# Performance work log

Hardware: AMD Instinct MI355X
Metric: run time of the kernel (lower is better)

The kernel has to match this reference:

```python
import jax, jax.numpy as jnp
import numpy as np

B, T, DIM = 256, 2048, 64
THETA, MU, SIGMA = 0.1, 0.0, 1.0


def setup_inputs() -> dict:
    key = jax.random.key(0)
    k1, k2 = jax.random.split(key)
    # strictly increasing positive times, shape [B, T, 1]
    dt = jax.random.uniform(k1, (B, T, 1), minval=1e-3, maxval=1e-2, dtype=jnp.float32)
    ts = jnp.cumsum(dt, axis=1)
    # standard normal reparameterization noise for Normal(0, delta_ts).rsample()
    noise = jax.random.normal(k2, (B, T, DIM), dtype=jnp.float32)
    return {"ts": ts, "noise": noise}


def reference(ts, noise):
    h = DIM // 2  # slice_index
    # t_prev: 0 at step 0, ts[:, :-1] afterwards
    t_prev = jnp.concatenate([jnp.zeros_like(ts[:, :1]), ts[:, :-1]], axis=1)  # [B,T,1]
    # Brownian-increment std: sqrt(t_k - t_{k-1})  (sqrt(t_0) at k=0)
    db = jnp.sqrt(ts - t_prev)  # [B,T,1]
    # OU-increment std: sqrt(exp(2*theta*t_k) - exp(2*theta*t_{k-1}))  (exp(0)=1 at k=0)
    dou = jnp.sqrt(jnp.exp(2.0 * THETA * ts) - jnp.exp(2.0 * THETA * t_prev))  # [B,T,1]
    bt = ts.shape[:-1]
    delta = jnp.concatenate([jnp.broadcast_to(db, bt + (h,)),
                             jnp.broadcast_to(dou, bt + (h,))], axis=-1)  # [B,T,DIM]
    invalid = delta <= 0.0
    delta = jnp.where(invalid, delta + 1e-4, delta)
    # rsample = 0 + delta * eps; zero out invalid entries
    r = jnp.where(invalid, 0.0, delta * noise)
    # per-half scaling
    scale = jnp.concatenate([jnp.full((h,), np.sqrt(SIGMA), dtype=r.dtype),
                             jnp.full((h,), SIGMA / np.sqrt(2.0 * THETA), dtype=r.dtype)])
    r = r * scale
    out = jnp.cumsum(r, axis=-2)  # scan along time
    # OU mean-reversion transform on second half
    e = jnp.exp(-THETA * ts)  # [B,T,1]
    ou = e * out[..., h:] + MU * (1.0 - e)
    # normalize=True branch
    bm = out[..., :h] / (SIGMA * jnp.sqrt(ts) + 1e-8)
    ou = ou / (SIGMA * jnp.sqrt((1.0 - jnp.exp(-2.0 * THETA * ts)) / (2.0 * THETA)) + 1e-8)
    return jnp.concatenate([bm, ou], axis=-1)  # [B,T,DIM]
```

## Files before the change

### kernel.cpp

```cpp
#include <hip/hip_runtime.h>
#include <cstddef>

#define B_   256
#define T_   2048
#define DIM_ 64
#define SGN_ 64
#define SPT_ (T_ / SGN_)
#define OU_SCALE 2.2360679774997896f

__global__ __launch_bounds__(1024) void fused_kernel(
        const float* __restrict__ ts,
        const float* __restrict__ noise,
        float* __restrict__ out)
{
    __shared__ float4 cofs[T_];
    __shared__ float4 par[SGN_][16];

    const int b   = blockIdx.x;
    const int tid = threadIdx.x;
    const int sg  = tid >> 4;
    const int qi  = tid & 15;
    const int q   = qi << 2;

    const float* tsb = ts + (size_t)b * T_;
    for (int t = tid; t < T_; t += 1024) {
        const float tk = tsb[t];
        const float tp = (t == 0) ? 0.0f : tsb[t - 1];
        const float dt = tk - tp;
        const float db  = sqrtf(dt);
        const float dou = sqrtf(expf(0.2f * tp) * expm1f(0.2f * dt));
        const float cb = (db  <= 0.0f) ? 0.0f : db;
        const float co = (dou <= 0.0f) ? 0.0f : dou * OU_SCALE;
        const float fb = 1.0f / (sqrtf(tk) + 1e-8f);
        const float em = expf(-0.1f * tk);
        const float fo = em / (sqrtf(-expm1f(-0.2f * tk) * 5.0f) + 1e-8f);
        cofs[t] = make_float4(cb, co, fb, fo);
    }
    __syncthreads();

    const size_t rowbase = (size_t)b * T_ * DIM_;
    const bool   ou      = q >= (DIM_ / 2);
    const int    tb      = sg * SPT_;
    const float* np = noise + rowbase + (size_t)tb * DIM_ + q;

    {
        float4 a = make_float4(0.f, 0.f, 0.f, 0.f);
#pragma unroll 8
        for (int i = 0; i < SPT_; ++i) {
            const float4 v = *(const float4*)(np + (size_t)i * DIM_);
            const float4 c = cofs[tb + i];
            const float  d = ou ? c.y : c.x;
            a.x = fmaf(d, v.x, a.x);
            a.y = fmaf(d, v.y, a.y);
            a.z = fmaf(d, v.z, a.z);
            a.w = fmaf(d, v.w, a.w);
        }
        par[sg][qi] = a;
    }
    __syncthreads();

    float4 acc = make_float4(0.f, 0.f, 0.f, 0.f);
    for (int k = 0; k < sg; ++k) {
        const float4 p = par[k][qi];
        acc.x += p.x; acc.y += p.y; acc.z += p.z; acc.w += p.w;
    }

    float* op = out + rowbase + (size_t)tb * DIM_ + q;
#pragma unroll 8
    for (int i = 0; i < SPT_; ++i) {
        const float4 v = *(const float4*)(np + (size_t)i * DIM_);
        const float4 c = cofs[tb + i];
        const float  d = ou ? c.y : c.x;
        const float  f = ou ? c.w : c.z;
        acc.x = fmaf(d, v.x, acc.x);
        acc.y = fmaf(d, v.y, acc.y);
        acc.z = fmaf(d, v.z, acc.z);
        acc.w = fmaf(d, v.w, acc.w);
        *(float4*)(op + (size_t)i * DIM_) =
            make_float4(acc.x * f, acc.y * f, acc.z * f, acc.w * f);
    }
}

extern "C" void kernel_launch(void* const* d_in, const int* in_sizes, int n_in,
                              void* d_out, int out_size, void* d_ws, size_t ws_size,
                              hipStream_t stream) {
    const float* ts    = (const float*)d_in[0];
    const float* noise = (const float*)d_in[1];
    float* out = (float*)d_out;
    (void)d_ws; (void)ws_size; (void)in_sizes; (void)n_in; (void)out_size;

    fused_kernel<<<B_, 1024, 0, stream>>>(ts, noise, out);
}
```

Measured before the change: 258.5 us.

## Split each batch row across two blocks by channel half with finer time segments

Launches two blocks per batch row, one for the Brownian half and one for the OU half of the channels. Each block computes only its own half's coefficients, stored as float2, which halves shared memory and removes the per-element select. Time is cut into 128 segments of 16 steps, with fully unrolled loops, so each block gets more parallelism and the grid covers the GPU better. The cost is that both blocks of a row recompute the ts loads and run their own prefix over 128 partials, and the prefix loop is longer.

```diff
diff --git a/kernel.cpp b/kernel.cpp
--- a/kernel.cpp
+++ b/kernel.cpp
@@ -4,52 +4,56 @@
 #define B_   256
 #define T_   2048
 #define DIM_ 64
-#define SGN_ 64
+#define HD_  (DIM_ / 2)
+#define SGN_ 128
 #define SPT_ (T_ / SGN_)
 #define OU_SCALE 2.2360679774997896f
 
-__global__ __launch_bounds__(1024) void fused_kernel(
+__global__ __launch_bounds__(1024, 8) void fused_kernel(
         const float* __restrict__ ts,
         const float* __restrict__ noise,
         float* __restrict__ out)
 {
-    __shared__ float4 cofs[T_];
-    __shared__ float4 par[SGN_][16];
+    __shared__ float2 cofs[T_];
+    __shared__ float4 par[SGN_][8];
 
-    const int b   = blockIdx.x;
+    const int bid = blockIdx.x;
+    const int b   = bid >> 1;
+    const int h   = bid & 1;
     const int tid = threadIdx.x;
-    const int sg  = tid >> 4;
-    const int qi  = tid & 15;
-    const int q   = qi << 2;
+    const int sg  = tid >> 3;
+    const int qi  = tid & 7;
+    const int q   = (h << 5) + (qi << 2);
 
     const float* tsb = ts + (size_t)b * T_;
     for (int t = tid; t < T_; t += 1024) {
         const float tk = tsb[t];
         const float tp = (t == 0) ? 0.0f : tsb[t - 1];
-        const float dt = tk - tp;
-        const float db  = sqrtf(dt);
-        const float dou = sqrtf(expf(0.2f * tp) * expm1f(0.2f * dt));
-        const float cb = (db  <= 0.0f) ? 0.0f : db;
-        const float co = (dou <= 0.0f) ? 0.0f : dou * OU_SCALE;
-        const float fb = 1.0f / (sqrtf(tk) + 1e-8f);
-        const float em = expf(-0.1f * tk);
-        const float fo = em / (sqrtf(-expm1f(-0.2f * tk) * 5.0f) + 1e-8f);
-        cofs[t] = make_float4(cb, co, fb, fo);
+        float d, f;
+        if (h == 0) {
+            const float db = sqrtf(tk - tp);
+            d = (db <= 0.0f) ? 0.0f : db;
+            f = 1.0f / (sqrtf(tk) + 1e-8f);
+        } else {
+            const float dou = sqrtf(expf(0.2f * tp) * expm1f(0.2f * (tk - tp)));
+            d = (dou <= 0.0f) ? 0.0f : dou * OU_SCALE;
+            const float em = expf(-0.1f * tk);
+            f = em / (sqrtf(-expm1f(-0.2f * tk) * 5.0f) + 1e-8f);
+        }
+        cofs[t] = make_float2(d, f);
     }
     __syncthreads();
 
     const size_t rowbase = (size_t)b * T_ * DIM_;
-    const bool   ou      = q >= (DIM_ / 2);
     const int    tb      = sg * SPT_;
     const float* np = noise + rowbase + (size_t)tb * DIM_ + q;
 
     {
         float4 a = make_float4(0.f, 0.f, 0.f, 0.f);
-#pragma unroll 8
+#pragma unroll
         for (int i = 0; i < SPT_; ++i) {
             const float4 v = *(const float4*)(np + (size_t)i * DIM_);
-            const float4 c = cofs[tb + i];
-            const float  d = ou ? c.y : c.x;
+            const float  d = cofs[tb + i].x;
             a.x = fmaf(d, v.x, a.x);
             a.y = fmaf(d, v.y, a.y);
             a.z = fmaf(d, v.z, a.z);
@@ -66,18 +70,16 @@
     }
 
     float* op = out + rowbase + (size_t)tb * DIM_ + q;
-#pragma unroll 8
+#pragma unroll
     for (int i = 0; i < SPT_; ++i) {
         const float4 v = *(const float4*)(np + (size_t)i * DIM_);
-        const float4 c = cofs[tb + i];
-        const float  d = ou ? c.y : c.x;
-        const float  f = ou ? c.w : c.z;
-        acc.x = fmaf(d, v.x, acc.x);
-        acc.y = fmaf(d, v.y, acc.y);
-        acc.z = fmaf(d, v.z, acc.z);
-        acc.w = fmaf(d, v.w, acc.w);
+        const float2 c = cofs[tb + i];
+        acc.x = fmaf(c.x, v.x, acc.x);
+        acc.y = fmaf(c.x, v.y, acc.y);
+        acc.z = fmaf(c.x, v.z, acc.z);
+        acc.w = fmaf(c.x, v.w, acc.w);
         *(float4*)(op + (size_t)i * DIM_) =
-            make_float4(acc.x * f, acc.y * f, acc.z * f, acc.w * f);
+            make_float4(acc.x * c.y, acc.y * c.y, acc.z * c.y, acc.w * c.y);
     }
 }
 
@@ -89,5 +91,5 @@
     float* out = (float*)d_out;
     (void)d_ws; (void)ws_size; (void)in_sizes; (void)n_in; (void)out_size;
 
-    fused_kernel<<<B_, 1024, 0, stream>>>(ts, noise, out);
+    fused_kernel<<<B_ * 2, 1024, 0, stream>>>(ts, noise, out);
 }
```

After: 251.9 us. 2.5% less time.
